# Optimization experiments

Measured on AMD Instinct MI355X. Metric: run time of the kernel, lower is better.

The kernel has to match this reference:

```python
import jax, jax.numpy as jnp
import numpy as np

B, L, D, E = 32, 2048, 1024, 2048

def setup_inputs() -> dict:
    key = jax.random.key(0)
    k1, k2, k3, k4, k5 = jax.random.split(key, 5)
    scale_s = 1.0 / np.sqrt(D)
    scale_h = 1.0 / np.sqrt(E)
    return {
        "dec_hidden": jax.random.normal(k1, (B, D), jnp.float32),
        "enc_outputs": jax.random.normal(k2, (B, L, E), jnp.float32),
        "W_s": jax.random.normal(k3, (D, D), jnp.float32) * scale_s,
        "W_h": jax.random.normal(k4, (D, E), jnp.float32) * scale_h,
        "v": jax.random.normal(k5, (D,), jnp.float32) * scale_s,
    }

def reference(dec_hidden, enc_outputs, W_s, W_h, v):
    # s: [B, D] -- projected decoder state (broadcast over src_len, no repeat)
    s = jnp.einsum('bd,ed->be', dec_hidden, W_s)
    # h: [B, L, D] -- projected encoder outputs
    h = jnp.einsum('ble,de->bld', enc_outputs, W_h)
    # additive scores: v^T tanh(s + h) -> [B, L]
    scores = jnp.einsum('bld,d->bl', jnp.tanh(s[:, None, :] + h), v)
    attn = jax.nn.softmax(scores, axis=1)
    # context: weighted sum of encoder outputs -> [B, E]
    ctx = jnp.einsum('bl,ble->be', attn, enc_outputs)
    return (ctx, attn)
```

## Files before the change

kernel.cpp:

```cpp
#include <hip/hip_runtime.h>
#include <cstdint>
#include <cstddef>

#define B_ 32
#define L_ 2048
#define D_ 1024
#define E_ 2048

typedef __attribute__((ext_vector_type(8))) short short8;
typedef __attribute__((ext_vector_type(16))) float f32x16;
typedef __attribute__((ext_vector_type(4))) unsigned int uint4v;

__device__ __forceinline__ unsigned int pack_bf16_2(float lo, float hi) {
  unsigned int ul = __builtin_bit_cast(unsigned int, lo) + 0x8000u;
  unsigned int uh = __builtin_bit_cast(unsigned int, hi) + 0x8000u;
  return (ul >> 16) | (uh & 0xFFFF0000u);
}

__device__ __forceinline__ unsigned int cvt_pk_bf16(float lo, float hi) {
  unsigned int r;
  asm("v_cvt_pk_bf16_f32 %0, %1, %2" : "=v"(r) : "v"(lo), "v"(hi));
  return r;
}

__device__ __forceinline__ float fast_tanh(float x) {
  float e = __expf(2.0f * x);
  return 1.0f - 2.0f / (e + 1.0f);
}

__global__ __launch_bounds__(256) void k_s(const float* __restrict__ dec,
                                           const float* __restrict__ Ws,
                                           float* __restrict__ s) {
  int wid = threadIdx.x >> 6, lane = threadIdx.x & 63;
  int out = blockIdx.x * 4 + wid;
  int b = out >> 10, i = out & 1023;
  const float* dr = dec + b * D_;
  const float* wr = Ws + (size_t)i * D_;
  float acc = 0.f;
#pragma unroll
  for (int c = 0; c < 4; ++c) {
    int d0 = c * 256 + lane * 4;
    float4 x = *(const float4*)(dr + d0);
    float4 w = *(const float4*)(wr + d0);
    acc += x.x * w.x + x.y * w.y + x.z * w.z + x.w * w.w;
  }
#pragma unroll
  for (int off = 32; off >= 1; off >>= 1) acc += __shfl_xor(acc, off, 64);
  if (lane == 0) s[out] = acc;
}

__global__ __launch_bounds__(256) void k_cvt(const float* __restrict__ src,
                                             unsigned short* __restrict__ dst) {
  size_t i = ((size_t)blockIdx.x * 256 + threadIdx.x) * 8;
  float4 a = *(const float4*)(src + i);
  float4 b = *(const float4*)(src + i + 4);
  uint4v p;
  p.x = pack_bf16_2(a.x, a.y);
  p.y = pack_bf16_2(a.z, a.w);
  p.z = pack_bf16_2(b.x, b.y);
  p.w = pack_bf16_2(b.z, b.w);
  *(uint4v*)(dst + i) = p;
}

__global__ __launch_bounds__(256, 2) void k_gemm(const float* __restrict__ enc,
                                                 const unsigned short* __restrict__ whb,
                                                 const float* __restrict__ sbias,
                                                 const float* __restrict__ vvec,
                                                 float* __restrict__ scores) {
  __shared__ alignas(16) unsigned short As[2][64 * 128];
  __shared__ alignas(16) unsigned short Bs[2][64 * 128];

  const int tid = threadIdx.x;
  const int wid = tid >> 6;
  const int lane = tid & 63;
  const int wm = wid >> 1;
  const int wn = wid & 1;

  const int flat = blockIdx.x;
  const int nt = (flat >> 3) & 7;
  const int mt = (flat & 7) | ((flat >> 6) << 3);
  const int m_base = mt * 128, n_base = nt * 128;
  const int b_idx = m_base >> 11;

  const int aRow = lane >> 4;
  const int aG = lane & 15;
  const float* gAr = enc + (size_t)(m_base + wid * 32 + aRow) * E_ + aG * 4;
  const int aUl = (aRow & 1) * 8 + (aG >> 1);
  const int aBy = (aG & 1) * 8;
  int aWoff[8];
#pragma unroll
  for (int i = 0; i < 8; ++i) {
    int line = wid * 16 + i * 2 + (aRow >> 1);
    aWoff[i] = line * 256 + ((aUl ^ (line & 15)) << 4) + aBy;
  }

  const int rp = lane >> 4;
  const int u0 = (lane & 15) ^ rp;
  const unsigned short* gB = whb + (size_t)n_base * E_;
  int offB[4], ldsB[4];
#pragma unroll
  for (int it = 0; it < 4; ++it) {
    int ulog = u0 ^ (it << 2);
    offB[it] = (wid * 32 + it * 8 + 2 * rp + (ulog >> 3)) * E_ + (ulog & 7) * 8;
    ldsB[it] = (wid * 16 + it * 4) * 256 + lane * 16;
  }

  const int col = lane & 31;
  const int h = lane >> 5;
  int soff[4];
#pragma unroll
  for (int ks = 0; ks < 4; ++ks)
    soff[ks] = ((((col & 1) << 3) + ks * 2 + h) ^ ((col >> 1) & 15)) << 4;
  int aOff[2], bOff[2];
#pragma unroll
  for (int mi = 0; mi < 2; ++mi) aOff[mi] = (wm * 32 + mi * 16 + (col >> 1)) * 256;
#pragma unroll
  for (int ni = 0; ni < 2; ++ni) bOff[ni] = (wn * 32 + ni * 16 + (col >> 1)) * 256;

  f32x16 acc[2][2] = {};
  float4 rAv0[8], rAv1[8];
  uint4v rBv[4];

#pragma unroll
  for (int it = 0; it < 4; ++it)
    rBv[it] = *(const uint4v*)(gB + offB[it]);
#pragma unroll
  for (int i = 0; i < 8; ++i)
    rAv0[i] = *(const float4*)(gAr + (size_t)(i * 4) * E_);
#pragma unroll
  for (int i = 0; i < 8; ++i)
    rAv1[i] = *(const float4*)(gAr + (size_t)(i * 4) * E_ + 64);
  {
    uint2 qa[8];
#pragma unroll
    for (int i = 0; i < 8; ++i) {
      qa[i].x = cvt_pk_bf16(rAv0[i].x, rAv0[i].y);
      qa[i].y = cvt_pk_bf16(rAv0[i].z, rAv0[i].w);
    }
#pragma unroll
    for (int i = 0; i < 8; ++i)
      *(uint2*)((char*)As + aWoff[i]) = qa[i];
#pragma unroll
    for (int it = 0; it < 4; ++it)
      *(uint4v*)((char*)Bs + ldsB[it]) = rBv[it];
  }
#pragma unroll
  for (int it = 0; it < 4; ++it)
    rBv[it] = *(const uint4v*)(gB + offB[it] + 64);
#pragma unroll
  for (int i = 0; i < 8; ++i)
    rAv0[i] = *(const float4*)(gAr + (size_t)(i * 4) * E_ + 128);
  asm volatile("s_waitcnt lgkmcnt(0)" ::: "memory");
  __builtin_amdgcn_sched_barrier(0);
  __builtin_amdgcn_s_barrier();
  __builtin_amdgcn_sched_barrier(0);

#define GSTEP(KK, RA, DO_PACK, DO_A, DO_B, RD)                              \
  {                                                                         \
    if (DO_PACK) {                                                          \
      uint2 qa[8];                                                          \
      _Pragma("unroll") for (int i = 0; i < 8; ++i) {                       \
        qa[i].x = cvt_pk_bf16(RA[i].x, RA[i].y);                            \
        qa[i].y = cvt_pk_bf16(RA[i].z, RA[i].w);                            \
      }                                                                     \
      _Pragma("unroll") for (int i = 0; i < 8; ++i)                         \
        *(uint2*)((char*)As + ((RD) ^ 16384) + aWoff[i]) = qa[i];           \
      _Pragma("unroll") for (int it = 0; it < 4; ++it)                      \
        *(uint4v*)((char*)Bs + ((RD) ^ 16384) + ldsB[it]) = rBv[it];        \
    }                                                                       \
    if (DO_B) {                                                             \
      _Pragma("unroll") for (int it = 0; it < 4; ++it)                      \
        rBv[it] = *(const uint4v*)(gB + offB[it] + (KK) + 128);             \
    }                                                                       \
    if (DO_A) {                                                             \
      _Pragma("unroll") for (int i = 0; i < 8; ++i)                         \
        RA[i] = *(const float4*)(gAr + (size_t)(i * 4) * E_ + (KK) + 192);  \
    }                                                                       \
    _Pragma("unroll") for (int ks = 0; ks < 4; ++ks) {                      \
      short8 bf[2], af[2];                                                  \
      _Pragma("unroll") for (int ni = 0; ni < 2; ++ni)                      \
        bf[ni] = *(const short8*)((char*)Bs + (RD) + bOff[ni] + soff[ks]);  \
      _Pragma("unroll") for (int mi = 0; mi < 2; ++mi)                      \
        af[mi] = *(const short8*)((char*)As + (RD) + aOff[mi] + soff[ks]);  \
      _Pragma("unroll") for (int mi = 0; mi < 2; ++mi)                      \
        _Pragma("unroll") for (int ni = 0; ni < 2; ++ni)                    \
          acc[mi][ni] = __builtin_amdgcn_mfma_f32_32x32x16_bf16(            \
              af[mi], bf[ni], acc[mi][ni], 0, 0, 0);                        \
    }                                                                       \
    asm volatile("s_waitcnt lgkmcnt(0)" ::: "memory");                      \
    __builtin_amdgcn_sched_barrier(0);                                      \
    __builtin_amdgcn_s_barrier();                                           \
    __builtin_amdgcn_sched_barrier(0);                                      \
  }

  for (int kk = 0; kk < 1792; kk += 128) {
    GSTEP(kk, rAv1, 1, 1, 1, 0);
    GSTEP(kk + 64, rAv0, 1, 1, 1, 16384);
  }
  GSTEP(1792, rAv1, 1, 1, 1, 0);
  GSTEP(1856, rAv0, 1, 0, 1, 16384);
  GSTEP(1920, rAv1, 1, 0, 0, 0);
  GSTEP(1984, rAv0, 0, 0, 0, 16384);
#undef GSTEP

  float vv[2], sv[2];
#pragma unroll
  for (int ni = 0; ni < 2; ++ni) {
    int n = n_base + wn * 64 + ni * 32 + col;
    vv[ni] = vvec[n];
    sv[ni] = sbias[b_idx * D_ + n];
  }
#pragma unroll
  for (int mi = 0; mi < 2; ++mi) {
#pragma unroll
    for (int reg = 0; reg < 16; ++reg) {
      float sum = 0.f;
#pragma unroll
      for (int ni = 0; ni < 2; ++ni)
        sum += vv[ni] * fast_tanh(sv[ni] + acc[mi][ni][reg]);
      sum += __shfl_xor(sum, 1, 64);
      sum += __shfl_xor(sum, 2, 64);
      sum += __shfl_xor(sum, 4, 64);
      sum += __shfl_xor(sum, 8, 64);
      sum += __shfl_xor(sum, 16, 64);
      if (col == 0)
        atomicAdd(&scores[m_base + wm * 64 + mi * 32 + (reg & 3) + 8 * (reg >> 2) + h * 4], sum);
    }
  }
}

__global__ __launch_bounds__(256) void k_softmax(float* __restrict__ sc) {
  int b = blockIdx.x, tid = threadIdx.x;
  int lane = tid & 63, wid = tid >> 6;
  float* row = sc + (size_t)b * L_;
  float vals[8];
  float mx = -1e30f;
#pragma unroll
  for (int j = 0; j < 8; ++j) { vals[j] = row[tid + j * 256]; mx = fmaxf(mx, vals[j]); }
#pragma unroll
  for (int off = 32; off >= 1; off >>= 1) mx = fmaxf(mx, __shfl_xor(mx, off, 64));
  __shared__ float redm[4], reds[4];
  if (lane == 0) redm[wid] = mx;
  __syncthreads();
  mx = fmaxf(fmaxf(redm[0], redm[1]), fmaxf(redm[2], redm[3]));
  float sum = 0.f;
#pragma unroll
  for (int j = 0; j < 8; ++j) { vals[j] = __expf(vals[j] - mx); sum += vals[j]; }
#pragma unroll
  for (int off = 32; off >= 1; off >>= 1) sum += __shfl_xor(sum, off, 64);
  if (lane == 0) reds[wid] = sum;
  __syncthreads();
  sum = reds[0] + reds[1] + reds[2] + reds[3];
  float inv = 1.0f / sum;
#pragma unroll
  for (int j = 0; j < 8; ++j) row[tid + j * 256] = vals[j] * inv;
}

__global__ __launch_bounds__(256) void k_ctx_p(const float* __restrict__ enc,
                                               const float* __restrict__ attn,
                                               float* __restrict__ partial) {
  int b = blockIdx.y;
  int lc = blockIdx.x >> 1;
  int eh = blockIdx.x & 1;
  int t = threadIdx.x;
  __shared__ float aw[128];
  if (t < 128) aw[t] = attn[(size_t)b * L_ + lc * 128 + t];
  __syncthreads();
  const float* base = enc + ((size_t)b * L_ + (size_t)lc * 128) * E_ + eh * 1024;
  float4 a0 = make_float4(0.f, 0.f, 0.f, 0.f);
#pragma unroll 8
  for (int l = 0; l < 128; ++l) {
    float w = aw[l];
    float4 x0 = *(const float4*)(base + (size_t)l * E_ + t * 4);
    a0.x += w * x0.x; a0.y += w * x0.y; a0.z += w * x0.z; a0.w += w * x0.w;
  }
  *(float4*)(partial + ((size_t)(lc * 32 + b) * E_) + eh * 1024 + t * 4) = a0;
}

__global__ __launch_bounds__(256) void k_ctx_r(const float* __restrict__ partial,
                                               float* __restrict__ ctx) {
  int idx = blockIdx.x * 256 + threadIdx.x;
  int b = idx >> 9;
  int e4 = idx & 511;
  float4 s = make_float4(0.f, 0.f, 0.f, 0.f);
#pragma unroll
  for (int c = 0; c < 16; ++c) {
    float4 p = *(const float4*)(partial + ((size_t)(c * 32 + b) * E_) + e4 * 4);
    s.x += p.x; s.y += p.y; s.z += p.z; s.w += p.w;
  }
  *(float4*)(ctx + (size_t)b * E_ + e4 * 4) = s;
}

extern "C" void kernel_launch(void* const* d_in, const int* in_sizes, int n_in,
                              void* d_out, int out_size, void* d_ws, size_t ws_size,
                              hipStream_t stream) {
  const float* dec = (const float*)d_in[0];
  const float* enc = (const float*)d_in[1];
  const float* Ws  = (const float*)d_in[2];
  const float* Wh  = (const float*)d_in[3];
  const float* v   = (const float*)d_in[4];

  float* ctx  = (float*)d_out;
  float* attn = (float*)d_out + B_ * E_;

  unsigned short* whb = (unsigned short*)d_ws;
  float* partial = (float*)d_ws;
  float* sbuf = (float*)((char*)d_ws + (size_t)D_ * E_ * sizeof(unsigned short));

  hipMemsetAsync(d_out, 0, (size_t)out_size * sizeof(float), stream);

  k_s<<<dim3((B_ * D_) / 4), dim3(256), 0, stream>>>(dec, Ws, sbuf);
  k_cvt<<<dim3((D_ * E_) / (256 * 8)), dim3(256), 0, stream>>>(Wh, whb);
  k_gemm<<<dim3((B_ * L_ / 128) * (D_ / 128)), dim3(256), 0, stream>>>(enc, whb, sbuf, v, attn);
  k_softmax<<<dim3(B_), dim3(256), 0, stream>>>(attn);
  k_ctx_p<<<dim3(32, B_), dim3(256), 0, stream>>>(enc, attn, partial);
  k_ctx_r<<<dim3((B_ * E_) / (256 * 4)), dim3(256), 0, stream>>>(partial, ctx);
}
```

Measured before the change: 1.065 ms.

## Halve GEMM K-tile to 32 and raise occupancy to three blocks per CU

The fused score GEMM's K step drops from 64 to 32. This halves the LDS buffers and the register staging arrays, and the launch bound moves from 2 to 3 blocks per CU to get more waves resident. The global-to-LDS load mapping is rebuilt so each thread pair loads one row contiguously, with a new XOR swizzle and new MFMA read offsets. The trade-off is twice as many barriers and loop iterations per tile, and fewer MFMAs between each sync.

```diff
diff --git a/kernel.cpp b/kernel.cpp
--- a/kernel.cpp
+++ b/kernel.cpp
@@ -62,13 +62,13 @@
   *(uint4v*)(dst + i) = p;
 }
 
-__global__ __launch_bounds__(256, 2) void k_gemm(const float* __restrict__ enc,
+__global__ __launch_bounds__(256, 3) void k_gemm(const float* __restrict__ enc,
                                                  const unsigned short* __restrict__ whb,
                                                  const float* __restrict__ sbias,
                                                  const float* __restrict__ vvec,
                                                  float* __restrict__ scores) {
-  __shared__ alignas(16) unsigned short As[2][64 * 128];
-  __shared__ alignas(16) unsigned short Bs[2][64 * 128];
+  __shared__ alignas(16) unsigned short As[2][32 * 128];
+  __shared__ alignas(16) unsigned short Bs[2][32 * 128];
 
   const int tid = threadIdx.x;
   const int wid = tid >> 6;
@@ -82,74 +82,72 @@
   const int m_base = mt * 128, n_base = nt * 128;
   const int b_idx = m_base >> 11;
 
-  const int aRow = lane >> 4;
-  const int aG = lane & 15;
-  const float* gAr = enc + (size_t)(m_base + wid * 32 + aRow) * E_ + aG * 4;
-  const int aUl = (aRow & 1) * 8 + (aG >> 1);
-  const int aBy = (aG & 1) * 8;
-  int aWoff[8];
-#pragma unroll
-  for (int i = 0; i < 8; ++i) {
-    int line = wid * 16 + i * 2 + (aRow >> 1);
-    aWoff[i] = line * 256 + ((aUl ^ (line & 15)) << 4) + aBy;
-  }
-
-  const int rp = lane >> 4;
-  const int u0 = (lane & 15) ^ rp;
-  const unsigned short* gB = whb + (size_t)n_base * E_;
-  int offB[4], ldsB[4];
-#pragma unroll
-  for (int it = 0; it < 4; ++it) {
-    int ulog = u0 ^ (it << 2);
-    offB[it] = (wid * 32 + it * 8 + 2 * rp + (ulog >> 3)) * E_ + (ulog & 7) * 8;
-    ldsB[it] = (wid * 16 + it * 4) * 256 + lane * 16;
-  }
+  const int tOdd = tid & 1;
+  const float* gAr = enc + (size_t)(m_base + (tid >> 1)) * E_ + tOdd * 4;
+  const int sLine = tid >> 3;
+  const int sR2 = (tid >> 1) & 3;
+  int aWoff[4];
+#pragma unroll
+  for (int c = 0; c < 4; ++c)
+    aWoff[c] = sLine * 256 + (((sR2 * 4 + c) ^ (sLine & 15)) << 4) + tOdd * 8;
+
+  const unsigned short* gBr = whb + (size_t)(n_base + (tid >> 1)) * E_ + tOdd * 8;
+  int bWoff[2];
+#pragma unroll
+  for (int j = 0; j < 2; ++j)
+    bWoff[j] = sLine * 256 + (((sR2 * 4 + 2 * j + tOdd) ^ (sLine & 15)) << 4);
 
   const int col = lane & 31;
   const int h = lane >> 5;
-  int soff[4];
-#pragma unroll
-  for (int ks = 0; ks < 4; ++ks)
-    soff[ks] = ((((col & 1) << 3) + ks * 2 + h) ^ ((col >> 1) & 15)) << 4;
-  int aOff[2], bOff[2];
-#pragma unroll
-  for (int mi = 0; mi < 2; ++mi) aOff[mi] = (wm * 32 + mi * 16 + (col >> 1)) * 256;
-#pragma unroll
-  for (int ni = 0; ni < 2; ++ni) bOff[ni] = (wn * 32 + ni * 16 + (col >> 1)) * 256;
+  int aRd[2][2], bRd[2][2];
+#pragma unroll
+  for (int mi = 0; mi < 2; ++mi)
+#pragma unroll
+    for (int ks = 0; ks < 2; ++ks) {
+      int line = wm * 16 + mi * 8 + (col >> 2);
+      int ul = (col & 3) * 4 + ks * 2 + h;
+      aRd[mi][ks] = line * 256 + ((ul ^ (line & 15)) << 4);
+    }
+#pragma unroll
+  for (int ni = 0; ni < 2; ++ni)
+#pragma unroll
+    for (int ks = 0; ks < 2; ++ks) {
+      int line = wn * 16 + ni * 8 + (col >> 2);
+      int ul = (col & 3) * 4 + ks * 2 + h;
+      bRd[ni][ks] = line * 256 + ((ul ^ (line & 15)) << 4);
+    }
 
   f32x16 acc[2][2] = {};
-  float4 rAv0[8], rAv1[8];
-  uint4v rBv[4];
-
-#pragma unroll
-  for (int it = 0; it < 4; ++it)
-    rBv[it] = *(const uint4v*)(gB + offB[it]);
-#pragma unroll
-  for (int i = 0; i < 8; ++i)
-    rAv0[i] = *(const float4*)(gAr + (size_t)(i * 4) * E_);
-#pragma unroll
-  for (int i = 0; i < 8; ++i)
-    rAv1[i] = *(const float4*)(gAr + (size_t)(i * 4) * E_ + 64);
+  float4 rAv0[4], rAv1[4];
+  uint4v rBv[2];
+
+#pragma unroll
+  for (int j = 0; j < 2; ++j)
+    rBv[j] = *(const uint4v*)(gBr + j * 16);
+#pragma unroll
+  for (int c = 0; c < 4; ++c)
+    rAv0[c] = *(const float4*)(gAr + c * 8);
+#pragma unroll
+  for (int c = 0; c < 4; ++c)
+    rAv1[c] = *(const float4*)(gAr + c * 8 + 32);
   {
-    uint2 qa[8];
-#pragma unroll
-    for (int i = 0; i < 8; ++i) {
-      qa[i].x = cvt_pk_bf16(rAv0[i].x, rAv0[i].y);
-      qa[i].y = cvt_pk_bf16(rAv0[i].z, rAv0[i].w);
+#pragma unroll
+    for (int c = 0; c < 4; ++c) {
+      uint2 qa;
+      qa.x = cvt_pk_bf16(rAv0[c].x, rAv0[c].y);
+      qa.y = cvt_pk_bf16(rAv0[c].z, rAv0[c].w);
+      *(uint2*)((char*)As + aWoff[c]) = qa;
     }
 #pragma unroll
-    for (int i = 0; i < 8; ++i)
-      *(uint2*)((char*)As + aWoff[i]) = qa[i];
-#pragma unroll
-    for (int it = 0; it < 4; ++it)
-      *(uint4v*)((char*)Bs + ldsB[it]) = rBv[it];
-  }
-#pragma unroll
-  for (int it = 0; it < 4; ++it)
-    rBv[it] = *(const uint4v*)(gB + offB[it] + 64);
-#pragma unroll
-  for (int i = 0; i < 8; ++i)
-    rAv0[i] = *(const float4*)(gAr + (size_t)(i * 4) * E_ + 128);
+    for (int j = 0; j < 2; ++j)
+      *(uint4v*)((char*)Bs + bWoff[j]) = rBv[j];
+  }
+#pragma unroll
+  for (int j = 0; j < 2; ++j)
+    rBv[j] = *(const uint4v*)(gBr + j * 16 + 32);
+#pragma unroll
+  for (int c = 0; c < 4; ++c)
+    rAv0[c] = *(const float4*)(gAr + c * 8 + 64);
   asm volatile("s_waitcnt lgkmcnt(0)" ::: "memory");
   __builtin_amdgcn_sched_barrier(0);
   __builtin_amdgcn_s_barrier();
@@ -158,30 +156,29 @@
 #define GSTEP(KK, RA, DO_PACK, DO_A, DO_B, RD)                              \
   {                                                                         \
     if (DO_PACK) {                                                          \
-      uint2 qa[8];                                                          \
-      _Pragma("unroll") for (int i = 0; i < 8; ++i) {                       \
-        qa[i].x = cvt_pk_bf16(RA[i].x, RA[i].y);                            \
-        qa[i].y = cvt_pk_bf16(RA[i].z, RA[i].w);                            \
+      _Pragma("unroll") for (int c = 0; c < 4; ++c) {                       \
+        uint2 qa;                                                           \
+        qa.x = cvt_pk_bf16(RA[c].x, RA[c].y);                               \
+        qa.y = cvt_pk_bf16(RA[c].z, RA[c].w);                               \
+        *(uint2*)((char*)As + ((RD) ^ 8192) + aWoff[c]) = qa;               \
       }                                                                     \
-      _Pragma("unroll") for (int i = 0; i < 8; ++i)                         \
-        *(uint2*)((char*)As + ((RD) ^ 16384) + aWoff[i]) = qa[i];           \
-      _Pragma("unroll") for (int it = 0; it < 4; ++it)                      \
-        *(uint4v*)((char*)Bs + ((RD) ^ 16384) + ldsB[it]) = rBv[it];        \
+      _Pragma("unroll") for (int j = 0; j < 2; ++j)                         \
+        *(uint4v*)((char*)Bs + ((RD) ^ 8192) + bWoff[j]) = rBv[j];          \
     }                                                                       \
     if (DO_B) {                                                             \
-      _Pragma("unroll") for (int it = 0; it < 4; ++it)                      \
-        rBv[it] = *(const uint4v*)(gB + offB[it] + (KK) + 128);             \
+      _Pragma("unroll") for (int j = 0; j < 2; ++j)                         \
+        rBv[j] = *(const uint4v*)(gBr + j * 16 + (KK) + 64);                \
     }                                                                       \
     if (DO_A) {                                                             \
-      _Pragma("unroll") for (int i = 0; i < 8; ++i)                         \
-        RA[i] = *(const float4*)(gAr + (size_t)(i * 4) * E_ + (KK) + 192);  \
+      _Pragma("unroll") for (int c = 0; c < 4; ++c)                         \
+        RA[c] = *(const float4*)(gAr + c * 8 + (KK) + 96);                  \
     }                                                                       \
-    _Pragma("unroll") for (int ks = 0; ks < 4; ++ks) {                      \
+    _Pragma("unroll") for (int ks = 0; ks < 2; ++ks) {                      \
       short8 bf[2], af[2];                                                  \
       _Pragma("unroll") for (int ni = 0; ni < 2; ++ni)                      \
-        bf[ni] = *(const short8*)((char*)Bs + (RD) + bOff[ni] + soff[ks]);  \
+        bf[ni] = *(const short8*)((char*)Bs + (RD) + bRd[ni][ks]);          \
       _Pragma("unroll") for (int mi = 0; mi < 2; ++mi)                      \
-        af[mi] = *(const short8*)((char*)As + (RD) + aOff[mi] + soff[ks]);  \
+        af[mi] = *(const short8*)((char*)As + (RD) + aRd[mi][ks]);          \
       _Pragma("unroll") for (int mi = 0; mi < 2; ++mi)                      \
         _Pragma("unroll") for (int ni = 0; ni < 2; ++ni)                    \
           acc[mi][ni] = __builtin_amdgcn_mfma_f32_32x32x16_bf16(            \
@@ -193,14 +190,14 @@
     __builtin_amdgcn_sched_barrier(0);                                      \
   }
 
-  for (int kk = 0; kk < 1792; kk += 128) {
+  for (int kk = 0; kk < 1920; kk += 64) {
     GSTEP(kk, rAv1, 1, 1, 1, 0);
-    GSTEP(kk + 64, rAv0, 1, 1, 1, 16384);
-  }
-  GSTEP(1792, rAv1, 1, 1, 1, 0);
-  GSTEP(1856, rAv0, 1, 0, 1, 16384);
-  GSTEP(1920, rAv1, 1, 0, 0, 0);
-  GSTEP(1984, rAv0, 0, 0, 0, 16384);
+    GSTEP(kk + 32, rAv0, 1, 1, 1, 8192);
+  }
+  GSTEP(1920, rAv1, 1, 1, 1, 0);
+  GSTEP(1952, rAv0, 1, 0, 1, 8192);
+  GSTEP(1984, rAv1, 1, 0, 0, 0);
+  GSTEP(2016, rAv0, 0, 0, 0, 8192);
 #undef GSTEP
 
   float vv[2], sv[2];
```

New measurement: 1.175 ms. +10.3%, slower.
